# Kernel optimization log

Hardware: AMD Instinct MI355X
Metric: run time of the kernel (lower is better)

The kernel has to match this reference:

```python
import jax, jax.numpy as jnp
import numpy as np

B, S, E, F, N = 2, 1024, 1024, 2048, 8


def setup_inputs() -> dict:
    key = jax.random.key(0)
    k0, k1, k2, k3, k4 = jax.random.split(key, 5)
    x = jax.random.normal(k0, (B, S, E), dtype=jnp.float32)
    # fan_in-scaled params, matching nd_dense_init(1.0, 'fan_in', ...)
    gate_kernel = jax.random.normal(k1, (E, N), dtype=jnp.float32) / np.sqrt(E).astype(np.float32)
    w0 = jax.random.normal(k2, (N, E, F), dtype=jnp.float32) / np.sqrt(E).astype(np.float32)
    w1 = jax.random.normal(k3, (N, E, F), dtype=jnp.float32) / np.sqrt(E).astype(np.float32)
    wo = jax.random.normal(k4, (N, F, E), dtype=jnp.float32) / np.sqrt(F).astype(np.float32)
    return {"x": x, "gate_kernel": gate_kernel, "w0": w0, "w1": w1, "wo": wo, "top_k": 2}


def reference(x, gate_kernel, w0, w1, wo, top_k):
    # x: [B, S, E] -> tokens [T, E]
    b, s, e = x.shape
    n = gate_kernel.shape[-1]
    xf = x.reshape(b * s, e)
    # Router: gate logits + top-k expert selection, softmax over top-k (fp32, as in permute())
    logits = jnp.einsum('te,en->tn', xf, gate_kernel)
    top_w, top_e = jax.lax.top_k(logits, top_k)               # [T, K]
    probs = jax.nn.softmax(top_w.astype(jnp.float32), axis=-1)  # [T, K]
    # Combine weights per (token, expert): scatter top-k probs into [T, N]
    combine = jnp.einsum('tk,tkn->tn', probs, jax.nn.one_hot(top_e, n, dtype=jnp.float32))
    # Expert FFN (dropless): h = silu(x@w0) * (x@w1); out_e = h @ wo   (same math as gmm path)
    h0 = jnp.einsum('te,nef->ntf', xf, w0)                    # [N, T, F]
    h1 = jnp.einsum('te,nef->ntf', xf, w1)
    h = jax.nn.silu(h0) * h1
    expert_out = jnp.einsum('ntf,nfe->nte', h, wo)            # [N, T, E]
    # Weighted combine over experts (matches unpermute's 'BKE,BK->BE' in fp32)
    out = jnp.einsum('nte,tn->te', expert_out, combine)
    return out.reshape(b, s, e)
```

## Files before the change

kernel.cpp:

```cpp
#include <hip/hip_runtime.h>
#include <hip/hip_bf16.h>

#define T_TOK 2048
#define E_DIM 1024
#define F_DIM 2048
#define N_EXP 8

typedef __attribute__((ext_vector_type(8))) short short8;
typedef __attribute__((ext_vector_type(4))) float f32x4;

__device__ __forceinline__ short bf2s(__hip_bfloat16 v) {
  union { __hip_bfloat16 b; short s; } u; u.b = v; return u.s;
}

__device__ __forceinline__ void gload_lds16(const void* g, void* l) {
  __builtin_amdgcn_global_load_lds((const __attribute__((address_space(1))) void*)g,
                                   (__attribute__((address_space(3))) void*)l, 16, 0, 0);
}

__device__ __forceinline__ void transpose_tile65(const float* __restrict__ src,
                                                 __hip_bfloat16* __restrict__ dst,
                                                 int C, int R, int r0, int c0,
                                                 int tt, float* lt) {
#pragma unroll
  for (int i = 0; i < 4; i++) {
    int chunk = i * 256 + tt;
    int r = chunk >> 4, c4 = (chunk & 15) * 4;
    float4 v = *(const float4*)(src + (size_t)(r0 + r) * C + c0 + c4);
    float* p = &lt[r * 65 + c4];
    p[0] = v.x; p[1] = v.y; p[2] = v.z; p[3] = v.w;
  }
  __syncthreads();
#pragma unroll
  for (int i = 0; i < 2; i++) {
    int chunk = i * 256 + tt;
    int c = chunk >> 3, rr = (chunk & 7) * 8;
    short8 o;
#pragma unroll
    for (int j = 0; j < 8; j++) o[j] = bf2s(__float2bfloat16(lt[(rr + j) * 65 + c]));
    *(short8*)(dst + (size_t)(c0 + c) * R + r0 + rr) = o;
  }
}

__global__ __launch_bounds__(256) void prep3d_kernel(const float* __restrict__ w0,
                                                     const float* __restrict__ w1,
                                                     const float* __restrict__ x,
                                                     const float* __restrict__ gk,
                                                     __hip_bfloat16* __restrict__ w0t,
                                                     __hip_bfloat16* __restrict__ w1t,
                                                     __hip_bfloat16* __restrict__ xb,
                                                     int* __restrict__ tk_e,
                                                     float* __restrict__ tk_p,
                                                     int* __restrict__ counts) {
  __shared__ float lt[64 * 65];
  int z = blockIdx.z;
  int tid = threadIdx.x;
  if (z < 16) {
    int e = z & 7;
    const float* src = (z < 8 ? w0 : w1) + (size_t)e * E_DIM * F_DIM;
    __hip_bfloat16* dst = (z < 8 ? w0t : w1t) + (size_t)e * E_DIM * F_DIM;
    transpose_tile65(src, dst, F_DIM, E_DIM, blockIdx.y * 64, blockIdx.x * 64, tid, lt);
    return;
  }
  int idx = blockIdx.y * 32 + blockIdx.x;
  if (z == 17) {
#pragma unroll
    for (int pass = 0; pass < 2; ++pass) {
      size_t i = (size_t)idx * 4096 + pass * 2048 + tid * 8;
      float4 a = *(const float4*)(x + i);
      float4 b = *(const float4*)(x + i + 4);
      short8 oo;
      oo[0] = bf2s(__float2bfloat16(a.x)); oo[1] = bf2s(__float2bfloat16(a.y));
      oo[2] = bf2s(__float2bfloat16(a.z)); oo[3] = bf2s(__float2bfloat16(a.w));
      oo[4] = bf2s(__float2bfloat16(b.x)); oo[5] = bf2s(__float2bfloat16(b.y));
      oo[6] = bf2s(__float2bfloat16(b.z)); oo[7] = bf2s(__float2bfloat16(b.w));
      *(short8*)(xb + i) = oo;
    }
    return;
  }
  int w = tid >> 6, l = tid & 63;
  int t = idx * 4 + w;
  const float* xr = x + (size_t)t * E_DIM;
  double acc[N_EXP];
#pragma unroll
  for (int n = 0; n < N_EXP; n++) acc[n] = 0.0;
  for (int j = 0; j < 16; j++) {
    int i = j * 64 + l;
    double xv = (double)xr[i];
    const float* g = gk + (size_t)i * N_EXP;
#pragma unroll
    for (int n = 0; n < N_EXP; n++) acc[n] += xv * (double)g[n];
  }
#pragma unroll
  for (int off = 32; off > 0; off >>= 1) {
#pragma unroll
    for (int n = 0; n < N_EXP; n++) acc[n] += __shfl_down(acc[n], off);
  }
  if (l == 0) {
    int e1 = 0; double v1 = acc[0];
    for (int n = 1; n < N_EXP; n++) if (acc[n] > v1) { v1 = acc[n]; e1 = n; }
    int e2 = -1; double v2 = -1e300;
    for (int n = 0; n < N_EXP; n++) if (n != e1 && acc[n] > v2) { v2 = acc[n]; e2 = n; }
    float ex = __expf((float)(v2 - v1));
    float p1 = 1.f / (1.f + ex);
    float p2 = ex / (1.f + ex);
    tk_e[t * 2 + 0] = e1; tk_p[t * 2 + 0] = p1;
    tk_e[t * 2 + 1] = e2; tk_p[t * 2 + 1] = p2;
    atomicAdd(&counts[e1], 1);
    atomicAdd(&counts[e2], 1);
  }
}

__global__ __launch_bounds__(256) void scanperm_kernel(const int* __restrict__ tk_e,
                                                       const float* __restrict__ tk_p,
                                                       int* __restrict__ ctrl,
                                                       int* __restrict__ slot_tok,
                                                       float* __restrict__ slot_prob,
                                                       int* __restrict__ inv) {
  __shared__ int offs[8], cur[8];
  int tid = threadIdx.x;
  if (tid == 0) {
    int off = 0, idx = 0;
    for (int e = 0; e < N_EXP; e++) {
      offs[e] = off; cur[e] = 0;
      int c = ctrl[e];
      for (int m0 = 0; m0 < c; m0 += 128) {
        ctrl[32 + idx] = e;
        ctrl[96 + idx] = off + m0;
        ctrl[160 + idx] = (c - m0 < 128) ? (c - m0) : 128;
        idx++;
      }
      off += c;
    }
    ctrl[24] = idx;
  }
  __syncthreads();
  for (int g = tid; g < 2 * T_TOK; g += 256) {
    int e = tk_e[g];
    float p = tk_p[g];
    int pos = atomicAdd(&cur[e], 1);
    int slot = offs[e] + pos;
    slot_tok[slot] = g >> 1;
    slot_prob[slot] = p;
    inv[g] = slot;
  }
}

__global__ __launch_bounds__(512, 4) void gemm1_kernel(const __hip_bfloat16* __restrict__ xb,
                                                       const __hip_bfloat16* __restrict__ w0t,
                                                       const __hip_bfloat16* __restrict__ w1t,
                                                       const int* __restrict__ ctrl,
                                                       const int* __restrict__ slot_tok,
                                                       __hip_bfloat16* __restrict__ h,
                                                       const float* __restrict__ wo,
                                                       __hip_bfloat16* __restrict__ wot) {
  __shared__ float ltf[2][64 * 65];
  short* lA  = (short*)&ltf[0][0];
  short* lB0 = lA + 8192;
  short* lB1 = lA + 12288;

  if (blockIdx.x >= 1280) {
    int half = threadIdx.x >> 8, tt = threadIdx.x & 255;
    int tile = (blockIdx.x - 1280) * 2 + half;
    int e = tile >> 9;
    int t2 = tile & 511;
    int r0 = (t2 & 31) * 64;
    int c0 = (t2 >> 5) * 64;
    transpose_tile65(wo + (size_t)e * F_DIM * E_DIM, wot + (size_t)e * E_DIM * F_DIM,
                     E_DIM, F_DIM, r0, c0, tt, &ltf[half][0]);
    return;
  }

  int lin = blockIdx.x;
  int logical = (lin & 7) * 160 + (lin >> 3);
  int mt = logical % 40;
  int fy = logical / 40;
  if (mt >= ctrl[24]) return;
  int e = ctrl[32 + mt];
  int slot0 = ctrl[96 + mt];
  int rowsv = ctrl[160 + mt];
  int f0 = fy * 64;

  int tid = threadIdx.x;
  int w = tid >> 6, l = tid & 63;
  int wm = w >> 1, wn = w & 1;
  int frow = l & 15, fk = l >> 4;

  int r1 = tid >> 3;
  int kc = ((tid & 7) ^ (r1 & 7)) * 8;
  int tokA1 = slot_tok[slot0 + r1];
  int tokA2 = slot_tok[slot0 + r1 + 64];
  const __hip_bfloat16* aS1 = xb + (size_t)tokA1 * E_DIM + kc;
  const __hip_bfloat16* aS2 = xb + (size_t)tokA2 * E_DIM + kc;
  const __hip_bfloat16* b0S = w0t + ((size_t)e * F_DIM + f0 + r1) * E_DIM + kc;
  const __hip_bfloat16* b1S = w1t + ((size_t)e * F_DIM + f0 + r1) * E_DIM + kc;

  f32x4 zero4 = {0.f, 0.f, 0.f, 0.f};
  f32x4 acc0[2][2], acc1[2][2];
#pragma unroll
  for (int mi = 0; mi < 2; mi++)
#pragma unroll
    for (int ni = 0; ni < 2; ni++) { acc0[mi][ni] = zero4; acc1[mi][ni] = zero4; }

  auto stage = [&](int t) {
    int k0 = t * 64;
    gload_lds16(aS1 + k0, &lA[w * 512]);
    gload_lds16(aS2 + k0, &lA[4096 + w * 512]);
    gload_lds16(b0S + k0, &lB0[w * 512]);
    gload_lds16(b1S + k0, &lB1[w * 512]);
  };

  const int NT = E_DIM / 64;
  for (int t = 0; t < NT; ++t) {
    if (t) __syncthreads();
    stage(t);
    __syncthreads();
    __builtin_amdgcn_s_setprio(1);
#pragma unroll
    for (int ks = 0; ks < 2; ++ks) {
      short8 a[2], b0[2], b1[2];
#pragma unroll
      for (int mi = 0; mi < 2; ++mi) {
        int r = wm * 32 + mi * 16 + frow;
        a[mi] = *(const short8*)&lA[r * 64 + ((ks * 4 + fk) ^ (r & 7)) * 8];
      }
#pragma unroll
      for (int ni = 0; ni < 2; ++ni) {
        int n = wn * 32 + ni * 16 + frow;
        int off = n * 64 + ((ks * 4 + fk) ^ (n & 7)) * 8;
        b0[ni] = *(const short8*)&lB0[off];
        b1[ni] = *(const short8*)&lB1[off];
      }
#pragma unroll
      for (int mi = 0; mi < 2; ++mi)
#pragma unroll
        for (int ni = 0; ni < 2; ++ni) {
          acc0[mi][ni] = __builtin_amdgcn_mfma_f32_16x16x32_bf16(a[mi], b0[ni], acc0[mi][ni], 0, 0, 0);
          acc1[mi][ni] = __builtin_amdgcn_mfma_f32_16x16x32_bf16(a[mi], b1[ni], acc1[mi][ni], 0, 0, 0);
        }
    }
    __builtin_amdgcn_s_setprio(0);
  }

#pragma unroll
  for (int mi = 0; mi < 2; ++mi) {
#pragma unroll
    for (int j = 0; j < 4; ++j) {
      int r = wm * 32 + mi * 16 + fk * 4 + j;
      if (r < rowsv) {
        __hip_bfloat16* hr = h + (size_t)(slot0 + r) * F_DIM + f0 + wn * 32;
#pragma unroll
        for (int ni = 0; ni < 2; ++ni) {
          float v0 = acc0[mi][ni][j];
          float v1 = acc1[mi][ni][j];
          float s = (v0 / (1.f + __expf(-v0))) * v1;
          hr[ni * 16 + frow] = __float2bfloat16(s);
        }
      }
    }
  }
}

__global__ __launch_bounds__(512, 4) void gemm2_kernel(const __hip_bfloat16* __restrict__ h,
                                                       const __hip_bfloat16* __restrict__ wot,
                                                       const int* __restrict__ ctrl,
                                                       const float* __restrict__ slot_prob,
                                                       float* __restrict__ parts) {
  int lin = blockIdx.x;
  int logical = (lin & 7) * 80 + (lin >> 3);
  int mt = logical % 40;
  int ey = logical / 40;
  if (mt >= ctrl[24]) return;
  int e = ctrl[32 + mt];
  int slot0 = ctrl[96 + mt];
  int rowsv = ctrl[160 + mt];
  int e0 = ey * 64;

  __shared__ alignas(16) short lA[128 * 64];
  __shared__ alignas(16) short lB[64 * 64];

  int tid = threadIdx.x;
  int w = tid >> 6, l = tid & 63;
  int wm = w >> 1, wn = w & 1;
  int frow = l & 15, fk = l >> 4;

  int r1 = tid >> 3;
  int kc = ((tid & 7) ^ (r1 & 7)) * 8;
  const __hip_bfloat16* aS1 = h + (size_t)(slot0 + r1) * F_DIM + kc;
  const __hip_bfloat16* aS2 = aS1 + (size_t)64 * F_DIM;
  const __hip_bfloat16* bS = wot + ((size_t)e * E_DIM + e0 + r1) * F_DIM + kc;

  f32x4 zero4 = {0.f, 0.f, 0.f, 0.f};
  f32x4 acc[2][2];
#pragma unroll
  for (int mi = 0; mi < 2; mi++)
#pragma unroll
    for (int ni = 0; ni < 2; ni++) acc[mi][ni] = zero4;

  auto stage = [&](int t) {
    int k0 = t * 64;
    gload_lds16(aS1 + k0, &lA[w * 512]);
    gload_lds16(aS2 + k0, &lA[4096 + w * 512]);
    gload_lds16(bS + k0, &lB[w * 512]);
  };

  const int NT = F_DIM / 64;
  for (int t = 0; t < NT; ++t) {
    if (t) __syncthreads();
    stage(t);
    __syncthreads();
    __builtin_amdgcn_s_setprio(1);
#pragma unroll
    for (int ks = 0; ks < 2; ++ks) {
      short8 a[2], b[2];
#pragma unroll
      for (int mi = 0; mi < 2; ++mi) {
        int r = wm * 32 + mi * 16 + frow;
        a[mi] = *(const short8*)&lA[r * 64 + ((ks * 4 + fk) ^ (r & 7)) * 8];
      }
#pragma unroll
      for (int ni = 0; ni < 2; ++ni) {
        int n = wn * 32 + ni * 16 + frow;
        b[ni] = *(const short8*)&lB[n * 64 + ((ks * 4 + fk) ^ (n & 7)) * 8];
      }
#pragma unroll
      for (int mi = 0; mi < 2; ++mi)
#pragma unroll
        for (int ni = 0; ni < 2; ++ni)
          acc[mi][ni] = __builtin_amdgcn_mfma_f32_16x16x32_bf16(a[mi], b[ni], acc[mi][ni], 0, 0, 0);
    }
    __builtin_amdgcn_s_setprio(0);
  }

#pragma unroll
  for (int mi = 0; mi < 2; ++mi) {
#pragma unroll
    for (int j = 0; j < 4; ++j) {
      int r = wm * 32 + mi * 16 + fk * 4 + j;
      if (r < rowsv) {
        int slot = slot0 + r;
        float p = slot_prob[slot];
        float* pr = parts + (size_t)slot * E_DIM + e0 + wn * 32;
#pragma unroll
        for (int ni = 0; ni < 2; ++ni)
          pr[ni * 16 + frow] = p * acc[mi][ni][j];
      }
    }
  }
}

__global__ __launch_bounds__(256) void combine_kernel(const float* __restrict__ parts,
                                                      const int* __restrict__ inv,
                                                      float* __restrict__ out) {
  int g = blockIdx.x * 256 + threadIdx.x;
  int row = g >> 7, c = (g & 127) * 8;
  int s1 = inv[row * 2], s2 = inv[row * 2 + 1];
  const float4* p1 = (const float4*)(parts + (size_t)s1 * E_DIM + c);
  const float4* p2 = (const float4*)(parts + (size_t)s2 * E_DIM + c);
  float4 a0 = p1[0], a1 = p1[1], b0 = p2[0], b1 = p2[1];
  float4 o0 = {a0.x + b0.x, a0.y + b0.y, a0.z + b0.z, a0.w + b0.w};
  float4 o1 = {a1.x + b1.x, a1.y + b1.y, a1.z + b1.z, a1.w + b1.w};
  float4* op = (float4*)(out + (size_t)row * E_DIM + c);
  op[0] = o0; op[1] = o1;
}

extern "C" void kernel_launch(void* const* d_in, const int* in_sizes, int n_in,
                              void* d_out, int out_size, void* d_ws, size_t ws_size,
                              hipStream_t stream) {
  const float* x  = (const float*)d_in[0];
  const float* gk = (const float*)d_in[1];
  const float* w0 = (const float*)d_in[2];
  const float* w1 = (const float*)d_in[3];
  const float* wo = (const float*)d_in[4];
  float* out = (float*)d_out;
  char* ws = (char*)d_ws;

  const size_t SLOTS = 2 * T_TOK + 128;
  const size_t OFF_XB   = 0;
  const size_t OFF_W0T  = OFF_XB  + (size_t)T_TOK * E_DIM * 2;
  const size_t OFF_W1T  = OFF_W0T + (size_t)N_EXP * E_DIM * F_DIM * 2;
  const size_t OFF_WOT  = OFF_W1T + (size_t)N_EXP * E_DIM * F_DIM * 2;
  const size_t OFF_H    = OFF_WOT + (size_t)N_EXP * F_DIM * E_DIM * 2;
  const size_t OFF_STOK = OFF_H   + SLOTS * F_DIM * 2;
  const size_t OFF_SPRB = OFF_STOK + SLOTS * 4;
  const size_t OFF_TKE  = OFF_SPRB + SLOTS * 4;
  const size_t OFF_TKP  = OFF_TKE + (size_t)2 * T_TOK * 4;
  const size_t OFF_INV  = OFF_TKP + (size_t)2 * T_TOK * 4;
  const size_t OFF_CTRL = OFF_INV + (size_t)2 * T_TOK * 4;
  const size_t NEED     = OFF_CTRL + 1024;
  if (ws_size < NEED) return;

  __hip_bfloat16* xb   = (__hip_bfloat16*)(ws + OFF_XB);
  __hip_bfloat16* w0t  = (__hip_bfloat16*)(ws + OFF_W0T);
  __hip_bfloat16* w1t  = (__hip_bfloat16*)(ws + OFF_W1T);
  __hip_bfloat16* wot  = (__hip_bfloat16*)(ws + OFF_WOT);
  __hip_bfloat16* hbuf = (__hip_bfloat16*)(ws + OFF_H);
  float* parts     = (float*)(ws + OFF_W0T);
  int*   slot_tok  = (int*)(ws + OFF_STOK);
  float* slot_prob = (float*)(ws + OFF_SPRB);
  int*   tk_e      = (int*)(ws + OFF_TKE);
  float* tk_p      = (float*)(ws + OFF_TKP);
  int*   inv       = (int*)(ws + OFF_INV);
  int*   ctrl      = (int*)(ws + OFF_CTRL);

  hipMemsetAsync(ctrl, 0, 1024, stream);
  hipMemsetAsync(slot_tok + 2 * T_TOK, 0, 128 * 4, stream);

  prep3d_kernel<<<dim3(32, 16, 18), 256, 0, stream>>>(w0, w1, x, gk, w0t, w1t, xb, tk_e, tk_p, ctrl);
  scanperm_kernel<<<1, 256, 0, stream>>>(tk_e, tk_p, ctrl, slot_tok, slot_prob, inv);
  gemm1_kernel<<<3328, 512, 0, stream>>>(xb, w0t, w1t, ctrl, slot_tok, hbuf, wo, wot);
  gemm2_kernel<<<640, 512, 0, stream>>>(hbuf, wot, ctrl, slot_prob, parts);
  combine_kernel<<<(T_TOK * 128) / 256, 256, 0, stream>>>(parts, inv, out);
}
```

Baseline: 210.3 us.

## Flatten prep grid and double-buffer weight transpose tiles per block

Replaces the 3D prep grid with a flat 1D grid where router/top-k blocks come first, x-conversion blocks next, and weight-transpose blocks last. Each transpose block now handles four 64x64 tiles, using a double-buffered LDS so the global loads for the next tile overlap the bf16 stores of the current one. The aim is to cut block count and scheduling overhead and to hide load latency in the memory-bound transpose. In exchange, LDS per block doubles and there are fewer blocks in flight.

```diff
diff --git a/kernel.cpp b/kernel.cpp
--- a/kernel.cpp
+++ b/kernel.cpp
@@ -42,28 +42,78 @@
   }
 }
 
-__global__ __launch_bounds__(256) void prep3d_kernel(const float* __restrict__ w0,
-                                                     const float* __restrict__ w1,
-                                                     const float* __restrict__ x,
-                                                     const float* __restrict__ gk,
-                                                     __hip_bfloat16* __restrict__ w0t,
-                                                     __hip_bfloat16* __restrict__ w1t,
-                                                     __hip_bfloat16* __restrict__ xb,
-                                                     int* __restrict__ tk_e,
-                                                     float* __restrict__ tk_p,
-                                                     int* __restrict__ counts) {
-  __shared__ float lt[64 * 65];
-  int z = blockIdx.z;
+__global__ __launch_bounds__(256) void prep_kernel(const float* __restrict__ w0,
+                                                   const float* __restrict__ w1,
+                                                   const float* __restrict__ x,
+                                                   const float* __restrict__ gk,
+                                                   __hip_bfloat16* __restrict__ w0t,
+                                                   __hip_bfloat16* __restrict__ w1t,
+                                                   __hip_bfloat16* __restrict__ xb,
+                                                   int* __restrict__ tk_e,
+                                                   float* __restrict__ tk_p,
+                                                   int* __restrict__ counts) {
+  __shared__ float lt[2][64 * 65];
+  int bid = blockIdx.x;
   int tid = threadIdx.x;
-  if (z < 16) {
-    int e = z & 7;
-    const float* src = (z < 8 ? w0 : w1) + (size_t)e * E_DIM * F_DIM;
-    __hip_bfloat16* dst = (z < 8 ? w0t : w1t) + (size_t)e * E_DIM * F_DIM;
-    transpose_tile65(src, dst, F_DIM, E_DIM, blockIdx.y * 64, blockIdx.x * 64, tid, lt);
+
+  if (bid >= 1024) {
+    int w = bid - 1024;
+    int which = w >> 10;
+    int rem = w & 1023;
+    int e = rem >> 7;
+    int rt = (rem >> 3) & 15;
+    int cq = rem & 7;
+    const float* src = (which ? w1 : w0) + (size_t)e * E_DIM * F_DIM;
+    __hip_bfloat16* dst = (which ? w1t : w0t) + (size_t)e * E_DIM * F_DIM;
+    int r0 = rt * 64;
+
+    float4 v[4];
+    auto loadT = [&](int i) {
+      int c0 = (cq * 4 + i) * 64;
+#pragma unroll
+      for (int k = 0; k < 4; k++) {
+        int chunk = k * 256 + tid;
+        int r = chunk >> 4, c4 = (chunk & 15) * 4;
+        v[k] = *(const float4*)(src + (size_t)(r0 + r) * F_DIM + c0 + c4);
+      }
+    };
+    auto wrLDS = [&](int b) {
+#pragma unroll
+      for (int k = 0; k < 4; k++) {
+        int chunk = k * 256 + tid;
+        int r = chunk >> 4, c4 = (chunk & 15) * 4;
+        float* p = &lt[b][r * 65 + c4];
+        p[0] = v[k].x; p[1] = v[k].y; p[2] = v[k].z; p[3] = v[k].w;
+      }
+    };
+    auto stphase = [&](int b, int i) {
+      int c0 = (cq * 4 + i) * 64;
+#pragma unroll
+      for (int k = 0; k < 2; k++) {
+        int chunk = k * 256 + tid;
+        int c = chunk >> 3, rr = (chunk & 7) * 8;
+        short8 o;
+#pragma unroll
+        for (int j = 0; j < 8; j++) o[j] = bf2s(__float2bfloat16(lt[b][(rr + j) * 65 + c]));
+        *(short8*)(dst + (size_t)(c0 + c) * E_DIM + r0 + rr) = o;
+      }
+    };
+
+    loadT(0);
+    wrLDS(0);
+#pragma unroll
+    for (int i = 0; i < 4; i++) {
+      int b = i & 1;
+      if (i < 3) loadT(i + 1);
+      __syncthreads();
+      stphase(b, i);
+      if (i < 3) wrLDS(b ^ 1);
+    }
     return;
   }
-  int idx = blockIdx.y * 32 + blockIdx.x;
-  if (z == 17) {
+
+  if (bid >= 512) {
+    int idx = bid - 512;
 #pragma unroll
     for (int pass = 0; pass < 2; ++pass) {
       size_t i = (size_t)idx * 4096 + pass * 2048 + tid * 8;
@@ -78,8 +128,9 @@
     }
     return;
   }
+
   int w = tid >> 6, l = tid & 63;
-  int t = idx * 4 + w;
+  int t = bid * 4 + w;
   const float* xr = x + (size_t)t * E_DIM;
   double acc[N_EXP];
 #pragma unroll
@@ -406,7 +457,7 @@
   hipMemsetAsync(ctrl, 0, 1024, stream);
   hipMemsetAsync(slot_tok + 2 * T_TOK, 0, 128 * 4, stream);
 
-  prep3d_kernel<<<dim3(32, 16, 18), 256, 0, stream>>>(w0, w1, x, gk, w0t, w1t, xb, tk_e, tk_p, ctrl);
+  prep_kernel<<<3072, 256, 0, stream>>>(w0, w1, x, gk, w0t, w1t, xb, tk_e, tk_p, ctrl);
   scanperm_kernel<<<1, 256, 0, stream>>>(tk_e, tk_p, ctrl, slot_tok, slot_prob, inv);
   gemm1_kernel<<<3328, 512, 0, stream>>>(xb, w0t, w1t, ctrl, slot_tok, hbuf, wo, wot);
   gemm2_kernel<<<640, 512, 0, stream>>>(hbuf, wot, ctrl, slot_prob, parts);
```

New measurement: 206.4 us. About the same (-1.9%).
